# Performance work log

Measured on AMD Instinct MI355X. Metric: run time of the kernel, lower is better.

The kernel has to match this reference:

```python
import jax, jax.numpy as jnp
import numpy as np

B, L, D, H, WIN, EXP = 2, 4096, 1024, 16, 256, 4

def setup_inputs() -> dict:
    key = jax.random.key(0)
    ks = jax.random.split(key, 8)
    F = EXP * D
    p = lambda k, shape: jax.random.normal(k, shape, dtype=jnp.float32) * 0.02
    return {
        "x": jax.random.normal(ks[0], (B, L, D), dtype=jnp.float32),
        "mask": jnp.zeros((B, L), dtype=jnp.float32),  # 0 = local attention everywhere
        "Wq": p(ks[1], (D, D)), "bq": jnp.zeros((D,), jnp.float32),
        "Wk": p(ks[2], (D, D)), "bk": jnp.zeros((D,), jnp.float32),
        "Wv": p(ks[3], (D, D)), "bv": jnp.zeros((D,), jnp.float32),
        "ln_g": jnp.ones((D,), jnp.float32), "ln_b": jnp.zeros((D,), jnp.float32),
        "W1": p(ks[4], (D, F)), "b1": jnp.zeros((F,), jnp.float32),
        "W2": p(ks[5], (F, D)), "b2": jnp.zeros((D,), jnp.float32),
    }


def reference(x, mask, Wq, bq, Wk, bk, Wv, bv, ln_g, ln_b, W1, b1, W2, b2):
    NEG = jnp.asarray(-1e9, x.dtype)
    Bs, Ls, Ds = x.shape
    dh = Ds // H
    c = WIN // 2  # one-sided window size (HF uses attention_window // 2)
    pad = WIN - Ls % WIN
    xp = jnp.pad(x, ((0, 0), (0, pad), (0, 0)))  # pad_token_id == 0
    mp = jnp.pad(mask, ((0, 0), (0, pad)), constant_values=-10000.0)
    S = Ls + pad
    n = S // c  # number of query chunks of size c

    inv_sqrt_dh = jnp.asarray(1.0 / np.sqrt(dh), x.dtype)
    q = ((xp @ Wq + bq) * inv_sqrt_dh).reshape(Bs, S, H, dh)
    k = (xp @ Wk + bk).reshape(Bs, S, H, dh)
    v = (xp @ Wv + bv).reshape(Bs, S, H, dh)

    # pad keys/values by one chunk on each side so query chunk i sees chunks i-1,i,i+1
    kp = jnp.pad(k, ((0, 0), (c, c), (0, 0), (0, 0)))
    vp = jnp.pad(v, ((0, 0), (c, c), (0, 0), (0, 0)))
    kvalid = jnp.pad(mp == 0.0, ((0, 0), (c, c)), constant_values=False)  # [B, S+2c]

    idx = jnp.arange(n)[:, None] * c + jnp.arange(3 * c)[None, :]  # [n, 3c]
    kc = kp[:, idx]   # [B, n, 3c, H, dh]
    vc = vp[:, idx]   # [B, n, 3c, H, dh]
    kvc = kvalid[:, idx]  # [B, n, 3c]
    qc = q.reshape(Bs, n, c, H, dh)

    scores = jnp.einsum('bnphd,bnrhd->bhnpr', qc, kc)  # [B,H,n,c,3c]
    p_ = jnp.arange(c)[:, None]
    r_ = jnp.arange(3 * c)[None, :]
    band = (r_ >= p_) & (r_ <= p_ + 2 * c)  # exact |i-j| <= c band, [c,3c]
    valid = band[None, None, None, :, :] & kvc[:, None, :, None, :]
    scores = jnp.where(valid, scores, NEG)
    probs = jax.nn.softmax(scores, axis=-1)
    attn = jnp.einsum('bhnpr,bnrhd->bnphd', probs, vc).reshape(Bs, S, Ds)

    h = (xp + attn)[:, :Ls]  # residual then drop padding (matches module order)
    mu = jnp.mean(h, axis=-1, keepdims=True)
    var = jnp.var(h, axis=-1, keepdims=True)
    h = (h - mu) / jnp.sqrt(var + 1e-5) * ln_g + ln_b
    out = h + (jax.nn.gelu(h @ W1 + b1, approximate=False) @ W2 + b2)
    return out
```

## Files before the change

kernel.cpp:

```cpp
#include <hip/hip_runtime.h>
#include <hip/hip_bf16.h>
#include <cstdint>

typedef __attribute__((ext_vector_type(8))) short short8;
typedef __attribute__((ext_vector_type(4))) short short4v;
typedef __attribute__((ext_vector_type(4))) float floatx4;

constexpr int B_ = 2, L_ = 4096, D_ = 1024, H_ = 16, DH = 64, F_ = 4096;
constexpr int M_ = B_ * L_;
constexpr int NQKV = 3 * D_;
constexpr int VT_GUARD = 512;

constexpr size_t OFF_XB  = 0;
constexpr size_t OFF_WCT = OFF_XB  + (size_t)M_ * D_ * 2;
constexpr size_t OFF_W1T = OFF_WCT + (size_t)NQKV * D_ * 2;
constexpr size_t OFF_W2T = OFF_W1T + (size_t)F_ * D_ * 2;
constexpr size_t OFF_QKV = OFF_W2T + (size_t)D_ * F_ * 2;
constexpr size_t OFF_VT  = OFF_QKV + (size_t)M_ * NQKV * 2;
constexpr size_t OFF_ATT = OFF_VT  + ((size_t)B_*H_*DH*L_ + 2*VT_GUARD) * 2;
constexpr size_t OFF_HB  = OFF_ATT + (size_t)M_ * D_ * 2;
constexpr size_t OFF_MID = OFF_HB  + (size_t)M_ * D_ * 2;

static __device__ __forceinline__ float b2f(unsigned short u) {
    union { unsigned int i; float f; } v; v.i = ((unsigned int)u) << 16; return v.f;
}

static __device__ __forceinline__ void gload16(const void* g, void* l) {
    __builtin_amdgcn_global_load_lds(
        (const __attribute__((address_space(1))) uint32_t*)g,
        (__attribute__((address_space(3))) uint32_t*)l, 16, 0, 0);
}

__global__ __launch_bounds__(256) void k_cvt_x(const float* __restrict__ x,
                                               __hip_bfloat16* __restrict__ xb) {
    int i = (blockIdx.x * 256 + threadIdx.x) * 8;
    float4 a = *(const float4*)(x + i);
    float4 b = *(const float4*)(x + i + 4);
    alignas(16) __hip_bfloat16 t[8];
    t[0] = __float2bfloat16(a.x); t[1] = __float2bfloat16(a.y);
    t[2] = __float2bfloat16(a.z); t[3] = __float2bfloat16(a.w);
    t[4] = __float2bfloat16(b.x); t[5] = __float2bfloat16(b.y);
    t[6] = __float2bfloat16(b.z); t[7] = __float2bfloat16(b.w);
    *(uint4*)(xb + i) = *(const uint4*)t;
}

__global__ __launch_bounds__(256) void k_tcvt(const float* __restrict__ in,
                                              __hip_bfloat16* __restrict__ out,
                                              int R, int C) {
    __shared__ float t[64][65];
    int tx = threadIdx.x & 63, ty4 = threadIdx.x >> 6;
    int c0 = blockIdx.x * 64, r0 = blockIdx.y * 64;
#pragma unroll
    for (int i = 0; i < 16; i++) {
        int r = ty4 + i * 4;
        t[r][tx] = in[(size_t)(r0 + r) * C + c0 + tx];
    }
    __syncthreads();
#pragma unroll
    for (int i = 0; i < 16; i++) {
        int r = ty4 + i * 4;
        out[(size_t)(c0 + r) * R + r0 + tx] = __float2bfloat16(t[tx][r]);
    }
}

__global__ __launch_bounds__(256) void k_vtrans(const __hip_bfloat16* __restrict__ qkv,
                                                __hip_bfloat16* __restrict__ vtg) {
    __shared__ __hip_bfloat16 t[64][72];
    int tx = threadIdx.x & 63, ty4 = threadIdx.x >> 6;
    int bh = blockIdx.y, b = bh >> 4, h = bh & 15;
    int j0 = blockIdx.x * 64;
#pragma unroll
    for (int i = 0; i < 16; i++) {
        int j = ty4 + i * 4;
        t[j][tx] = qkv[(size_t)(b * L_ + j0 + j) * NQKV + 2 * D_ + h * DH + tx];
    }
    __syncthreads();
#pragma unroll
    for (int i = 0; i < 16; i++) {
        int d = ty4 + i * 4;
        vtg[(long)(bh * DH + d) * L_ + j0 + tx] = t[tx][d];
    }
}

template<int NT, int WN, int GM, int EPI, int KTOT, int NBN, int MINW>
__global__ __launch_bounds__(NT, MINW)
void k_p3(const __hip_bfloat16* __restrict__ A, const __hip_bfloat16* __restrict__ BT,
          const float* __restrict__ b0p, const float* __restrict__ b1p,
          const float* __restrict__ b2p,
          __hip_bfloat16* __restrict__ obf, float* __restrict__ of32,
          const __hip_bfloat16* __restrict__ hres) {
    constexpr int BN = WN * 64;
    constexpr int KT = KTOT / 32;
    constexpr int PER = GM * NBN;
    constexpr int A_LOADS = (128 * 4) / NT;
    constexpr int B_LOADS = (BN * 4) / NT;
    constexpr int LPT = A_LOADS + B_LOADS;
    constexpr int RSWEEP = NT / 4;

    __shared__ __hip_bfloat16 AS[3][128 * 32];
    __shared__ __hip_bfloat16 BS[3][BN * 32];

    const int tid = threadIdx.x, wave = tid >> 6, lane = tid & 63;
    const int lo = lane & 15, hi = lane >> 4;
    const int wm = wave / WN, wn = wave % WN;

    const int nwg = gridDim.x, q = nwg >> 3;
    const int bid = blockIdx.x;
    const int swz = (bid & 7) * q + (bid >> 3);
    const int g = swz / PER, r = swz % PER;
    const int bm = g * GM + (r % GM);
    const int bn = r / GM;
    const size_t m0 = (size_t)bm * 128, n0 = (size_t)bn * BN;

    const int r0 = tid >> 2;
    const int gcc = (tid & 3) ^ (r0 & 3);
    const __hip_bfloat16* aG = A  + (m0 + r0) * (size_t)KTOT + gcc * 8;
    const __hip_bfloat16* bG = BT + (n0 + r0) * (size_t)KTOT + gcc * 8;

    const int cR = (hi ^ (lo & 3)) * 8;
    const int aOff = (wm * 64 + lo) * 32 + cR;
    const int bOff = (wn * 64 + lo) * 32 + cR;

    floatx4 acc[4][4] = {};

#define STAGE(buf, kt)                                                        \
    do {                                                                      \
        _Pragma("unroll")                                                     \
        for (int s = 0; s < A_LOADS; ++s)                                     \
            gload16(aG + (size_t)(s * RSWEEP) * KTOT + (size_t)(kt) * 32,     \
                    &AS[buf][(s * NT + wave * 64) * 8]);                      \
        _Pragma("unroll")                                                     \
        for (int s = 0; s < B_LOADS; ++s)                                     \
            gload16(bG + (size_t)(s * RSWEEP) * KTOT + (size_t)(kt) * 32,     \
                    &BS[buf][(s * NT + wave * 64) * 8]);                      \
    } while (0)

#define WAITVM_LPT()                                                          \
    do {                                                                      \
        if constexpr (LPT == 3) asm volatile("s_waitcnt vmcnt(3)" ::: "memory"); \
        else                    asm volatile("s_waitcnt vmcnt(4)" ::: "memory"); \
    } while (0)

    STAGE(0, 0);
    STAGE(1, 1);
    WAITVM_LPT();
    __builtin_amdgcn_sched_barrier(0);
    __builtin_amdgcn_s_barrier();

    int cur = 0, nb = 2;
    for (int t = 0; t < KT; ++t) {
        const int tf = (t + 2 < KT) ? (t + 2) : t;
        STAGE(nb, tf);

        const __hip_bfloat16* aL = &AS[cur][0];
        const __hip_bfloat16* bL = &BS[cur][0];
        short8 afr[4], bfr[4];
#pragma unroll
        for (int f = 0; f < 4; ++f) afr[f] = *(const short8*)(aL + aOff + f * 512);
#pragma unroll
        for (int f = 0; f < 4; ++f) bfr[f] = *(const short8*)(bL + bOff + f * 512);

        __builtin_amdgcn_s_setprio(1);
#pragma unroll
        for (int mf = 0; mf < 4; ++mf)
#pragma unroll
            for (int nf = 0; nf < 4; ++nf)
                acc[mf][nf] = __builtin_amdgcn_mfma_f32_16x16x32_bf16(
                    afr[mf], bfr[nf], acc[mf][nf], 0, 0, 0);
        __builtin_amdgcn_s_setprio(0);

        WAITVM_LPT();
        __builtin_amdgcn_sched_barrier(0);
        __builtin_amdgcn_s_barrier();

        cur = (cur == 2) ? 0 : cur + 1;
        nb  = (nb  == 2) ? 0 : nb  + 1;
    }
#undef STAGE
#undef WAITVM_LPT

#pragma unroll
    for (int mf = 0; mf < 4; ++mf) {
        const int row = (int)m0 + wm * 64 + mf * 16 + hi * 4;
#pragma unroll
        for (int nf = 0; nf < 4; ++nf) {
            const int col = (int)n0 + wn * 64 + nf * 16 + lo;
#pragma unroll
            for (int rr = 0; rr < 4; ++rr) {
                float v = acc[mf][nf][rr];
                const size_t ro = (size_t)(row + rr);
                if (EPI == 0) {
                    float bia = (col < 1024) ? b0p[col]
                              : (col < 2048 ? b1p[col - 1024] : b2p[col - 2048]);
                    obf[ro * NQKV + col] = __float2bfloat16(v + bia);
                } else if (EPI == 1) {
                    v += b0p[col];
                    v = 0.5f * v * (1.0f + erff(v * 0.70710678118654752440f));
                    obf[ro * F_ + col] = __float2bfloat16(v);
                } else {
                    v += b0p[col];
                    v += b2f(*(const unsigned short*)&hres[ro * D_ + col]);
                    of32[ro * D_ + col] = v;
                }
            }
        }
    }
}

__global__ __launch_bounds__(256, 2)
void k_attn(const __hip_bfloat16* __restrict__ qkv, const float* __restrict__ mask,
            const __hip_bfloat16* __restrict__ vtg, __hip_bfloat16* __restrict__ attnb) {
    constexpr int PS = 296;
    __shared__ __hip_bfloat16 P[4][16 * PS];
    const int tid = threadIdx.x, wave = tid >> 6, lane = tid & 63;
    const int bh = blockIdx.y, b = bh >> 4, h = bh & 15;
    const int q0 = blockIdx.x * 64 + wave * 16;
    const int lo = lane & 15, hi = lane >> 4;

    short8 qf0, qf1;
    {
        const __hip_bfloat16* qb = qkv + (size_t)(b * L_ + q0 + lo) * NQKV + h * DH + hi * 8;
        qf0 = *(const short8*)qb;
        qf1 = *(const short8*)(qb + 32);
    }

    floatx4 sc[17];
    const __hip_bfloat16* kcol = qkv + (size_t)b * L_ * NQKV + D_ + h * DH + hi * 8;
#pragma unroll
    for (int t = 0; t < 17; t++) {
        int jg = q0 - 128 + t * 16 + lo;
        int jc = jg < 0 ? 0 : (jg >= L_ ? L_ - 1 : jg);
        const __hip_bfloat16* kb = kcol + (size_t)jc * NQKV;
        short8 kf0 = *(const short8*)kb;
        short8 kf1 = *(const short8*)(kb + 32);
        floatx4 a = {};
        a = __builtin_amdgcn_mfma_f32_16x16x32_bf16(qf0, kf0, a, 0, 0, 0);
        a = __builtin_amdgcn_mfma_f32_16x16x32_bf16(qf1, kf1, a, 0, 0, 0);
        float mval = mask[b * L_ + jc];
        bool jok = (jg >= 0) && (jg < L_) && (mval == 0.0f);
#pragma unroll
        for (int r = 0; r < 4; r++) {
            int qi = q0 + hi * 4 + r;
            bool ok = jok && (jg >= qi - 128) && (jg <= qi + 128);
            a[r] = ok ? a[r] * 0.125f : -1e9f;
        }
        sc[t] = a;
    }

#pragma unroll
    for (int r = 0; r < 4; r++) {
        float m = -3e38f;
#pragma unroll
        for (int t = 0; t < 17; t++) m = fmaxf(m, sc[t][r]);
        m = fmaxf(m, __shfl_xor(m, 1));
        m = fmaxf(m, __shfl_xor(m, 2));
        m = fmaxf(m, __shfl_xor(m, 4));
        m = fmaxf(m, __shfl_xor(m, 8));
        float s = 0.0f;
#pragma unroll
        for (int t = 0; t < 17; t++) { float e = __expf(sc[t][r] - m); sc[t][r] = e; s += e; }
        s += __shfl_xor(s, 1); s += __shfl_xor(s, 2);
        s += __shfl_xor(s, 4); s += __shfl_xor(s, 8);
        float inv = 1.0f / s;
#pragma unroll
        for (int t = 0; t < 17; t++) sc[t][r] *= inv;
    }

    __hip_bfloat16* Pw = &P[wave][0];
#pragma unroll
    for (int t = 0; t < 17; t++)
#pragma unroll
        for (int r = 0; r < 4; r++)
            Pw[(hi * 4 + r) * PS + t * 16 + lo] = __float2bfloat16(sc[t][r]);
    {
        int zr = lane >> 2, zc = 272 + (lane & 3) * 4;
        __hip_bfloat16 z = __float2bfloat16(0.0f);
#pragma unroll
        for (int i = 0; i < 4; i++) Pw[zr * PS + zc + i] = z;
    }

    floatx4 o[4] = {};
#pragma unroll
    for (int st = 0; st < 9; st++) {
        short8 pa = *(const short8*)(Pw + lo * PS + st * 32 + hi * 8);
        int jb = q0 - 128 + st * 32 + hi * 8;
#pragma unroll
        for (int dt = 0; dt < 4; dt++) {
            const __hip_bfloat16* vb = vtg + (long)(bh * DH + dt * 16 + lo) * L_ + jb;
            short8 vf = *(const short8*)vb;
            o[dt] = __builtin_amdgcn_mfma_f32_16x16x32_bf16(pa, vf, o[dt], 0, 0, 0);
        }
    }

#pragma unroll
    for (int dt = 0; dt < 4; dt++)
#pragma unroll
        for (int r = 0; r < 4; r++) {
            int row = q0 + hi * 4 + r;
            attnb[(size_t)(b * L_ + row) * D_ + h * DH + dt * 16 + lo] =
                __float2bfloat16(o[dt][r]);
        }
}

__global__ __launch_bounds__(256)
void k_ln(const float* __restrict__ x, const __hip_bfloat16* __restrict__ attnb,
          const float* __restrict__ g, const float* __restrict__ bt,
          __hip_bfloat16* __restrict__ hb) {
    const int row = blockIdx.x, tid = threadIdx.x;
    const int c4 = tid * 4;
    float4 xv = *(const float4*)(x + (size_t)row * D_ + c4);
    short4v av = *(const short4v*)(attnb + (size_t)row * D_ + c4);
    float h0 = xv.x + b2f((unsigned short)av[0]);
    float h1 = xv.y + b2f((unsigned short)av[1]);
    float h2 = xv.z + b2f((unsigned short)av[2]);
    float h3 = xv.w + b2f((unsigned short)av[3]);
    float s = h0 + h1 + h2 + h3;
    float q = h0 * h0 + h1 * h1 + h2 * h2 + h3 * h3;
#pragma unroll
    for (int off = 32; off > 0; off >>= 1) {
        s += __shfl_down(s, off);
        q += __shfl_down(q, off);
    }
    __shared__ float red[8];
    int wave = tid >> 6, lane = tid & 63;
    if (lane == 0) { red[wave] = s; red[4 + wave] = q; }
    __syncthreads();
    s = red[0] + red[1] + red[2] + red[3];
    q = red[4] + red[5] + red[6] + red[7];
    float mu = s * (1.0f / D_);
    float var = q * (1.0f / D_) - mu * mu;
    float inv = rsqrtf(var + 1e-5f);
    float4 gv = *(const float4*)(g + c4);
    float4 bv = *(const float4*)(bt + c4);
    alignas(8) __hip_bfloat16 ov[4];
    ov[0] = __float2bfloat16((h0 - mu) * inv * gv.x + bv.x);
    ov[1] = __float2bfloat16((h1 - mu) * inv * gv.y + bv.y);
    ov[2] = __float2bfloat16((h2 - mu) * inv * gv.z + bv.z);
    ov[3] = __float2bfloat16((h3 - mu) * inv * gv.w + bv.w);
    *(short4v*)(hb + (size_t)row * D_ + c4) = *(const short4v*)ov;
}

extern "C" void kernel_launch(void* const* d_in, const int* in_sizes, int n_in,
                              void* d_out, int out_size, void* d_ws, size_t ws_size,
                              hipStream_t stream) {
    const float* x    = (const float*)d_in[0];
    const float* mask = (const float*)d_in[1];
    const float* Wq   = (const float*)d_in[2];
    const float* bq   = (const float*)d_in[3];
    const float* Wk   = (const float*)d_in[4];
    const float* bk   = (const float*)d_in[5];
    const float* Wv   = (const float*)d_in[6];
    const float* bv   = (const float*)d_in[7];
    const float* ln_g = (const float*)d_in[8];
    const float* ln_b = (const float*)d_in[9];
    const float* W1   = (const float*)d_in[10];
    const float* b1   = (const float*)d_in[11];
    const float* W2   = (const float*)d_in[12];
    const float* b2   = (const float*)d_in[13];
    float* out = (float*)d_out;
    char* ws = (char*)d_ws;

    __hip_bfloat16* xb   = (__hip_bfloat16*)(ws + OFF_XB);
    __hip_bfloat16* wct  = (__hip_bfloat16*)(ws + OFF_WCT);
    __hip_bfloat16* w1t  = (__hip_bfloat16*)(ws + OFF_W1T);
    __hip_bfloat16* w2t  = (__hip_bfloat16*)(ws + OFF_W2T);
    __hip_bfloat16* qkvb = (__hip_bfloat16*)(ws + OFF_QKV);
    __hip_bfloat16* vtg  = (__hip_bfloat16*)(ws + OFF_VT) + VT_GUARD;
    __hip_bfloat16* attb = (__hip_bfloat16*)(ws + OFF_ATT);
    __hip_bfloat16* hb   = (__hip_bfloat16*)(ws + OFF_HB);
    __hip_bfloat16* midb = (__hip_bfloat16*)(ws + OFF_MID);

    k_cvt_x<<<(M_ * D_) / 2048, 256, 0, stream>>>(x, xb);
    k_tcvt<<<dim3(D_ / 64, D_ / 64), 256, 0, stream>>>(Wq, wct,                   D_, D_);
    k_tcvt<<<dim3(D_ / 64, D_ / 64), 256, 0, stream>>>(Wk, wct + 1024 * 1024,     D_, D_);
    k_tcvt<<<dim3(D_ / 64, D_ / 64), 256, 0, stream>>>(Wv, wct + 2 * 1024 * 1024, D_, D_);
    k_tcvt<<<dim3(F_ / 64, D_ / 64), 256, 0, stream>>>(W1, w1t, D_, F_);
    k_tcvt<<<dim3(D_ / 64, F_ / 64), 256, 0, stream>>>(W2, w2t, F_, D_);

    k_p3<512, 4, 8, 0, D_, 12, 4><<<768, 512, 0, stream>>>(
        xb, wct, bq, bk, bv, qkvb, nullptr, nullptr);

    k_vtrans<<<dim3(L_ / 64, B_ * H_), 256, 0, stream>>>(qkvb, vtg);
    k_attn<<<dim3(L_ / 64, B_ * H_), 256, 0, stream>>>(qkvb, mask, vtg, attb);

    k_ln<<<M_, 256, 0, stream>>>(x, attb, ln_g, ln_b, hb);

    k_p3<512, 4, 8, 1, D_, 16, 4><<<1024, 512, 0, stream>>>(
        hb, w1t, b1, nullptr, nullptr, midb, nullptr, nullptr);
    k_p3<256, 2, 2, 2, F_, 8, 3><<<512, 256, 0, stream>>>(
        midb, w2t, b2, nullptr, nullptr, nullptr, out, hb);
}
```

Before: 490.3 us.

## Add 4-wave 128x256 GEMM kernel for QKV and FFN1, unroll triple-buffer loop

Adds a new GEMM kernel, k_w8, that uses 256 threads (4 waves) per 128x256 tile. Each wave computes a full 128x64 strip (8x4 MFMA fragments), so A fragments are reused across more MFMAs per LDS read. The QKV and W1 projections now use it in place of the 512-thread 4x4-fragment-per-wave kernel. The triple-buffer K loop is also unrolled by three so buffer indices are compile-time constants, in both the new kernel and k_p3. The cost is higher register pressure from 128 accumulator floats per lane, which may limit occupancy.

```diff
diff --git a/kernel.cpp b/kernel.cpp
--- a/kernel.cpp
+++ b/kernel.cpp
@@ -82,11 +82,124 @@
     }
 }
 
+template<int GM, int EPI, int NBN>
+__global__ __launch_bounds__(256, 2)
+void k_w8(const __hip_bfloat16* __restrict__ A, const __hip_bfloat16* __restrict__ BT,
+          const float* __restrict__ b0p, const float* __restrict__ b1p,
+          const float* __restrict__ b2p,
+          __hip_bfloat16* __restrict__ obf, float* __restrict__ of32) {
+    constexpr int KTOT = 1024;
+    constexpr int KT = KTOT / 32;
+    constexpr int PER = GM * NBN;
+
+    __shared__ __hip_bfloat16 AS[3][128 * 32];
+    __shared__ __hip_bfloat16 BS[3][256 * 32];
+
+    const int tid = threadIdx.x, wave = tid >> 6, lane = tid & 63;
+    const int lo = lane & 15, hi = lane >> 4;
+    const int wn = wave;
+
+    const int nwg = gridDim.x, q = nwg >> 3;
+    const int bid = blockIdx.x;
+    const int swz = (bid & 7) * q + (bid >> 3);
+    const int g = swz / PER, r = swz % PER;
+    const int bm = g * GM + (r % GM);
+    const int bn = r / GM;
+    const size_t m0 = (size_t)bm * 128, n0 = (size_t)bn * 256;
+
+    const int r0 = tid >> 2;
+    const int gcc = (tid & 3) ^ (r0 & 3);
+    const __hip_bfloat16* aG = A  + (m0 + r0) * (size_t)KTOT + gcc * 8;
+    const __hip_bfloat16* bG = BT + (n0 + r0) * (size_t)KTOT + gcc * 8;
+
+    const int cR = (hi ^ (lo & 3)) * 8;
+    const int aOff = lo * 32 + cR;
+    const int bOff = (wn * 64 + lo) * 32 + cR;
+
+    floatx4 acc[8][4] = {};
+
+#define STAGE(buf, kt)                                                        \
+    do {                                                                      \
+        _Pragma("unroll")                                                     \
+        for (int s = 0; s < 2; ++s)                                           \
+            gload16(aG + (size_t)(s * 64) * KTOT + (size_t)(kt) * 32,         \
+                    &AS[buf][(s * 256 + wave * 64) * 8]);                     \
+        _Pragma("unroll")                                                     \
+        for (int s = 0; s < 4; ++s)                                           \
+            gload16(bG + (size_t)(s * 64) * KTOT + (size_t)(kt) * 32,         \
+                    &BS[buf][(s * 256 + wave * 64) * 8]);                     \
+    } while (0)
+
+#define BODY(t, CUR, NB)                                                      \
+    do {                                                                      \
+        const int tf = ((t) + 2 < KT) ? (t) + 2 : (t);                        \
+        STAGE(NB, tf);                                                        \
+        short8 bfr[4], afr[8];                                                \
+        _Pragma("unroll")                                                     \
+        for (int gf = 0; gf < 4; ++gf)                                        \
+            bfr[gf] = *(const short8*)(&BS[CUR][0] + bOff + gf * 512);        \
+        _Pragma("unroll")                                                     \
+        for (int f = 0; f < 8; ++f)                                           \
+            afr[f] = *(const short8*)(&AS[CUR][0] + aOff + f * 512);          \
+        __builtin_amdgcn_s_setprio(1);                                        \
+        _Pragma("unroll")                                                     \
+        for (int mf = 0; mf < 8; ++mf)                                        \
+            _Pragma("unroll")                                                 \
+            for (int nf = 0; nf < 4; ++nf)                                    \
+                acc[mf][nf] = __builtin_amdgcn_mfma_f32_16x16x32_bf16(        \
+                    afr[mf], bfr[nf], acc[mf][nf], 0, 0, 0);                  \
+        __builtin_amdgcn_s_setprio(0);                                        \
+        asm volatile("s_waitcnt vmcnt(6)" ::: "memory");                      \
+        __builtin_amdgcn_sched_barrier(0);                                    \
+        __builtin_amdgcn_s_barrier();                                         \
+    } while (0)
+
+    STAGE(0, 0);
+    STAGE(1, 1);
+    asm volatile("s_waitcnt vmcnt(6)" ::: "memory");
+    __builtin_amdgcn_sched_barrier(0);
+    __builtin_amdgcn_s_barrier();
+
+#pragma unroll 1
+    for (int t = 0; t + 3 <= KT; t += 3) {
+        BODY(t,     0, 2);
+        BODY(t + 1, 1, 0);
+        BODY(t + 2, 2, 1);
+    }
+    BODY(KT - 2, 0, 2);
+    BODY(KT - 1, 1, 0);
+#undef STAGE
+#undef BODY
+
+#pragma unroll
+    for (int mf = 0; mf < 8; ++mf) {
+        const int row = (int)m0 + mf * 16 + hi * 4;
+#pragma unroll
+        for (int gf = 0; gf < 4; ++gf) {
+            const int col = (int)n0 + wn * 64 + gf * 16 + lo;
+#pragma unroll
+            for (int rr = 0; rr < 4; ++rr) {
+                float v = acc[mf][gf][rr];
+                const size_t ro = (size_t)(row + rr);
+                if (EPI == 0) {
+                    float bia = (col < 1024) ? b0p[col]
+                              : (col < 2048 ? b1p[col - 1024] : b2p[col - 2048]);
+                    obf[ro * NQKV + col] = __float2bfloat16(v + bia);
+                } else {
+                    v += b0p[col];
+                    v = 0.5f * v * (1.0f + erff(v * 0.70710678118654752440f));
+                    obf[ro * F_ + col] = __float2bfloat16(v);
+                }
+            }
+        }
+    }
+    (void)of32;
+}
+
 template<int NT, int WN, int GM, int EPI, int KTOT, int NBN, int MINW>
 __global__ __launch_bounds__(NT, MINW)
 void k_p3(const __hip_bfloat16* __restrict__ A, const __hip_bfloat16* __restrict__ BT,
-          const float* __restrict__ b0p, const float* __restrict__ b1p,
-          const float* __restrict__ b2p,
+          const float* __restrict__ b0p,
           __hip_bfloat16* __restrict__ obf, float* __restrict__ of32,
           const __hip_bfloat16* __restrict__ hres) {
     constexpr int BN = WN * 64;
@@ -141,43 +254,46 @@
         else                    asm volatile("s_waitcnt vmcnt(4)" ::: "memory"); \
     } while (0)
 
+#define BODY(t, CUR, NB)                                                      \
+    do {                                                                      \
+        const int tf = ((t) + 2 < KT) ? (t) + 2 : (t);                        \
+        STAGE(NB, tf);                                                        \
+        short8 afr[4], bfr[4];                                                \
+        _Pragma("unroll")                                                     \
+        for (int f = 0; f < 4; ++f) {                                         \
+            afr[f] = *(const short8*)(&AS[CUR][0] + aOff + f * 512);          \
+            bfr[f] = *(const short8*)(&BS[CUR][0] + bOff + f * 512);          \
+        }                                                                     \
+        __builtin_amdgcn_s_setprio(1);                                        \
+        _Pragma("unroll")                                                     \
+        for (int mf = 0; mf < 4; ++mf)                                        \
+            _Pragma("unroll")                                                 \
+            for (int nf = 0; nf < 4; ++nf)                                    \
+                acc[mf][nf] = __builtin_amdgcn_mfma_f32_16x16x32_bf16(        \
+                    afr[mf], bfr[nf], acc[mf][nf], 0, 0, 0);                  \
+        __builtin_amdgcn_s_setprio(0);                                        \
+        WAITVM_LPT();                                                         \
+        __builtin_amdgcn_sched_barrier(0);                                    \
+        __builtin_amdgcn_s_barrier();                                         \
+    } while (0)
+
     STAGE(0, 0);
     STAGE(1, 1);
     WAITVM_LPT();
     __builtin_amdgcn_sched_barrier(0);
     __builtin_amdgcn_s_barrier();
 
-    int cur = 0, nb = 2;
-    for (int t = 0; t < KT; ++t) {
-        const int tf = (t + 2 < KT) ? (t + 2) : t;
-        STAGE(nb, tf);
-
-        const __hip_bfloat16* aL = &AS[cur][0];
-        const __hip_bfloat16* bL = &BS[cur][0];
-        short8 afr[4], bfr[4];
-#pragma unroll
-        for (int f = 0; f < 4; ++f) afr[f] = *(const short8*)(aL + aOff + f * 512);
-#pragma unroll
-        for (int f = 0; f < 4; ++f) bfr[f] = *(const short8*)(bL + bOff + f * 512);
-
-        __builtin_amdgcn_s_setprio(1);
-#pragma unroll
-        for (int mf = 0; mf < 4; ++mf)
-#pragma unroll
-            for (int nf = 0; nf < 4; ++nf)
-                acc[mf][nf] = __builtin_amdgcn_mfma_f32_16x16x32_bf16(
-                    afr[mf], bfr[nf], acc[mf][nf], 0, 0, 0);
-        __builtin_amdgcn_s_setprio(0);
-
-        WAITVM_LPT();
-        __builtin_amdgcn_sched_barrier(0);
-        __builtin_amdgcn_s_barrier();
-
-        cur = (cur == 2) ? 0 : cur + 1;
-        nb  = (nb  == 2) ? 0 : nb  + 1;
-    }
+#pragma unroll 1
+    for (int t = 0; t + 3 <= KT; t += 3) {
+        BODY(t,     0, 2);
+        BODY(t + 1, 1, 0);
+        BODY(t + 2, 2, 1);
+    }
+    BODY(KT - 2, 0, 2);
+    BODY(KT - 1, 1, 0);
 #undef STAGE
 #undef WAITVM_LPT
+#undef BODY
 
 #pragma unroll
     for (int mf = 0; mf < 4; ++mf) {
@@ -189,22 +305,13 @@
             for (int rr = 0; rr < 4; ++rr) {
                 float v = acc[mf][nf][rr];
                 const size_t ro = (size_t)(row + rr);
-                if (EPI == 0) {
-                    float bia = (col < 1024) ? b0p[col]
-                              : (col < 2048 ? b1p[col - 1024] : b2p[col - 2048]);
-                    obf[ro * NQKV + col] = __float2bfloat16(v + bia);
-                } else if (EPI == 1) {
-                    v += b0p[col];
-                    v = 0.5f * v * (1.0f + erff(v * 0.70710678118654752440f));
-                    obf[ro * F_ + col] = __float2bfloat16(v);
-                } else {
-                    v += b0p[col];
-                    v += b2f(*(const unsigned short*)&hres[ro * D_ + col]);
-                    of32[ro * D_ + col] = v;
-                }
+                v += b0p[col];
+                v += b2f(*(const unsigned short*)&hres[ro * D_ + col]);
+                of32[ro * D_ + col] = v;
             }
         }
     }
+    (void)obf;
 }
 
 __global__ __launch_bounds__(256, 2)
@@ -377,16 +484,14 @@
     k_tcvt<<<dim3(F_ / 64, D_ / 64), 256, 0, stream>>>(W1, w1t, D_, F_);
     k_tcvt<<<dim3(D_ / 64, F_ / 64), 256, 0, stream>>>(W2, w2t, F_, D_);
 
-    k_p3<512, 4, 8, 0, D_, 12, 4><<<768, 512, 0, stream>>>(
-        xb, wct, bq, bk, bv, qkvb, nullptr, nullptr);
+    k_w8<8, 0, 12><<<768, 256, 0, stream>>>(xb, wct, bq, bk, bv, qkvb, nullptr);
 
     k_vtrans<<<dim3(L_ / 64, B_ * H_), 256, 0, stream>>>(qkvb, vtg);
     k_attn<<<dim3(L_ / 64, B_ * H_), 256, 0, stream>>>(qkvb, mask, vtg, attb);
 
     k_ln<<<M_, 256, 0, stream>>>(x, attb, ln_g, ln_b, hb);
 
-    k_p3<512, 4, 8, 1, D_, 16, 4><<<1024, 512, 0, stream>>>(
-        hb, w1t, b1, nullptr, nullptr, midb, nullptr, nullptr);
+    k_w8<8, 1, 16><<<1024, 256, 0, stream>>>(hb, w1t, b1, nullptr, nullptr, midb, nullptr);
     k_p3<256, 2, 2, 2, F_, 8, 3><<<512, 256, 0, stream>>>(
-        midb, w2t, b2, nullptr, nullptr, nullptr, out, hb);
-}
+        midb, w2t, b2, nullptr, out, hb);
+}
```

After: 501.3 us. 2.3% more time.
